# Kernel optimization log

Measured on AMD Instinct MI355X. Metric: run time of the kernel, lower is better.

Reference implementation:

```python
import jax, jax.numpy as jnp
import numpy as np

B, S, E = 2, 1024, 2048
NH = 8          # num attention heads
KVH = 1         # num key/value heads (GQA)
DH = E // NH    # head dim = 256
CAP = 15.0      # gate soft cap
EPS = 1e-6


def setup_inputs() -> dict:
    key = jax.random.key(0)
    ks = jax.random.split(key, 11)
    g = lambda k, shape, sc=0.02: (jax.random.normal(k, shape, jnp.float32) * sc)
    return {
        "x": jax.random.normal(ks[0], (B, S, E), jnp.float32),
        "Wq": g(ks[1], (E, NH * DH)),
        "Wk": g(ks[2], (E, KVH * DH)),
        "Wv": g(ks[3], (E, KVH * DH)),
        "Wog": g(ks[4], (E, E)),
        "Wi": g(ks[5], (E, NH)),
        "bi": g(ks[6], (NH,), 0.1),
        "Wf": g(ks[7], (E, NH)),
        "bf": jnp.ones((NH,), jnp.float32) * 2.0,  # bias forget gate open, as in xLSTM practice
        "gamma": jnp.ones((E,), jnp.float32),       # multihead layernorm weight
        "Wout": g(ks[8], (E, E)),
    }


def _soft_cap(z):
    return CAP * jnp.tanh(z / CAP)


def _repeat_kv(h, n_rep):
    # (B, KVH, S, DH) -> (B, KVH*n_rep, S, DH)
    if n_rep == 1:
        return h
    b, kvh, s, d = h.shape
    return jnp.broadcast_to(h[:, :, None], (b, kvh, n_rep, s, d)).reshape(b, kvh * n_rep, s, d)


def reference(x, Wq, Wk, Wv, Wog, Wi, bi, Wf, bf, gamma, Wout):
    # --- projections ---
    q = (x @ Wq).reshape(B, S, NH, DH).transpose(0, 2, 1, 3)          # (B,NH,S,DH)
    k = (x @ Wk).reshape(B, S, KVH, DH).transpose(0, 2, 1, 3)         # (B,KVH,S,DH)
    v = (x @ Wv).reshape(B, S, KVH, DH).transpose(0, 2, 1, 3)
    k = _repeat_kv(k, NH // KVH)
    v = _repeat_kv(v, NH // KVH)
    o_preact = x @ Wog                                                # (B,S,E)
    i_pre = _soft_cap(x @ Wi + bi).transpose(0, 2, 1)                 # (B,NH,S)
    f_pre = _soft_cap(x @ Wf + bf).transpose(0, 2, 1)                 # (B,NH,S)

    # --- parallel (stabilized) mLSTM backend ---
    logf = jax.nn.log_sigmoid(f_pre)
    cf = jnp.cumsum(logf, axis=-1)                                    # (B,NH,S)
    mat_logf = cf[:, :, :, None] - cf[:, :, None, :]                  # (B,NH,S,S)
    ltr = jnp.tril(jnp.ones((S, S), dtype=bool))
    mat_logD = jnp.where(ltr, mat_logf, -jnp.inf) + i_pre[:, :, None, :]
    vecM = jnp.max(mat_logD, axis=-1, keepdims=True)                  # (B,NH,S,1)
    matD = jnp.exp(mat_logD - vecM)
    matS = jnp.einsum('bhsd,bhtd->bhst', q, k) * (DH ** -0.5)
    matCt = matS * matD
    vecN = jnp.maximum(jnp.abs(matCt.sum(-1, keepdims=True)), jnp.exp(-vecM))
    matC = matCt / (vecN + EPS)
    h = jnp.einsum('bhst,bhtd->bhsd', matC, v)                        # (B,NH,S,DH)

    # --- multihead layernorm (per-head, float32 reductions) ---
    h = h.transpose(0, 2, 1, 3)                                       # (B,S,NH,DH)
    hf = h.astype(jnp.float32)
    mu = hf.mean(-1, keepdims=True)
    var = hf.var(-1, keepdims=True)
    h_norm = ((hf - mu) * jax.lax.rsqrt(var + EPS)).astype(h.dtype)
    h_norm = (h_norm * gamma.reshape(NH, DH)).reshape(B, S, E)

    # --- output gate + projection ---
    y = (jax.nn.sigmoid(o_preact) * h_norm) @ Wout
    return y
```

## Files before the change

kernel.cpp:

```cpp
#include <hip/hip_runtime.h>
#include <math.h>

#define S_LEN  1024
#define EMB    2048
#define NH_    8
#define DH_    256
#define TOKENS 2048
#define NBH    16
#define NQKVO  4608

typedef __attribute__((ext_vector_type(4))) float    f32x4;
typedef __attribute__((ext_vector_type(8))) _Float16 f16x8;
typedef __attribute__((ext_vector_type(4))) _Float16 f16x4;

__device__ __forceinline__ _Float16 f2h(float f) { return (_Float16)f; }

__device__ __forceinline__ void gload16(const void* g, void* l) {
  __builtin_amdgcn_global_load_lds(
      (const __attribute__((address_space(1))) void*)g,
      (__attribute__((address_space(3))) void*)l, 16, 0, 0);
}

__global__ __launch_bounds__(256) void prep_kernel(
    const float* __restrict__ x, const float* __restrict__ Wi, const float* __restrict__ bi,
    const float* __restrict__ Wf, const float* __restrict__ bfg,
    const float* __restrict__ Wq, const float* __restrict__ Wk,
    const float* __restrict__ Wv, const float* __restrict__ Wog,
    const float* __restrict__ Wout,
    _Float16* __restrict__ xh, float* __restrict__ ip, float* __restrict__ fp,
    _Float16* __restrict__ WcatT, _Float16* __restrict__ WoutT)
{
  __shared__ float shmem[64][65];
  int t = blockIdx.x;
  const int tid = threadIdx.x;
  if (t < TOKENS) {
    const int tok = t;
    const float* xr = x + (long)tok * EMB;
    float ai[8] = {}, af[8] = {};
    #pragma unroll
    for (int j = 0; j < 8; ++j) {
      const int e = tid + j * 256;
      const float xe = xr[e];
      xh[(long)tok * EMB + e] = f2h(xe);
      const float4* wi4 = (const float4*)(Wi + (long)e * 8);
      const float4* wf4 = (const float4*)(Wf + (long)e * 8);
      const float4 a0 = wi4[0], a1 = wi4[1], b0 = wf4[0], b1 = wf4[1];
      ai[0] += xe * a0.x; ai[1] += xe * a0.y; ai[2] += xe * a0.z; ai[3] += xe * a0.w;
      ai[4] += xe * a1.x; ai[5] += xe * a1.y; ai[6] += xe * a1.z; ai[7] += xe * a1.w;
      af[0] += xe * b0.x; af[1] += xe * b0.y; af[2] += xe * b0.z; af[3] += xe * b0.w;
      af[4] += xe * b1.x; af[5] += xe * b1.y; af[6] += xe * b1.z; af[7] += xe * b1.w;
    }
    #pragma unroll
    for (int hh = 0; hh < 8; ++hh)
      for (int off = 32; off; off >>= 1) {
        ai[hh] += __shfl_xor(ai[hh], off);
        af[hh] += __shfl_xor(af[hh], off);
      }
    float (*red)[16] = (float(*)[16])shmem;
    const int lane = tid & 63, wid = tid >> 6;
    if (lane == 0) {
      #pragma unroll
      for (int hh = 0; hh < 8; ++hh) { red[wid][hh] = ai[hh]; red[wid][hh + 8] = af[hh]; }
    }
    __syncthreads();
    if (tid < 16) {
      const float v = red[0][tid] + red[1][tid] + red[2][tid] + red[3][tid];
      const int b = tok >> 10, s = tok & 1023;
      if (tid < 8) {
        const float zv = v + bi[tid];
        ip[(long)(b * NH_ + tid) * S_LEN + s] = 15.0f * tanhf(zv * (1.0f / 15.0f));
      } else {
        const int hh = tid - 8;
        const float zv = v + bfg[hh];
        fp[(long)(b * NH_ + hh) * S_LEN + s] = 15.0f * tanhf(zv * (1.0f / 15.0f));
      }
    }
  } else {
    t -= TOKENS;
    const float* in; _Float16* out; int ldi, ct;
    if (t < 1024)      { in = Wq;   out = WcatT;                    ldi = 2048; ct = 32; }
    else if (t < 1152) { t -= 1024; in = Wk;  out = WcatT + (long)2048 * EMB; ldi = 256; ct = 4; }
    else if (t < 1280) { t -= 1152; in = Wv;  out = WcatT + (long)2304 * EMB; ldi = 256; ct = 4; }
    else if (t < 2304) { t -= 1280; in = Wog; out = WcatT + (long)2560 * EMB; ldi = 2048; ct = 32; }
    else               { t -= 2304; in = Wout; out = WoutT;         ldi = 2048; ct = 32; }
    const long c0 = (long)(t % ct) * 64, r0 = (long)(t / ct) * 64;
    const int lx = tid & 63, ly = tid >> 6;
    #pragma unroll
    for (int i = 0; i < 16; ++i)
      shmem[ly + i * 4][lx] = in[(r0 + ly + i * 4) * ldi + c0 + lx];
    __syncthreads();
    #pragma unroll
    for (int i = 0; i < 16; ++i)
      out[(c0 + ly + i * 4) * EMB + r0 + lx] = f2h(shmem[lx][ly + i * 4]);
  }
}

template<typename CT, int BM>
__global__ __launch_bounds__(256) void gemm_bt_kernel(
    const _Float16* __restrict__ Ag, const _Float16* __restrict__ Btg,
    CT* __restrict__ Cg, int K, int lda, int ldb, int ldc,
    long sA, long sB, long sC, int zdivB, int mtiles, int causal)
{
  constexpr int MR = BM / 32;
  __shared__ _Float16 As[3][BM * 32];
  __shared__ _Float16 Bs[3][128 * 32];
  const int tid = threadIdx.x;
  const int lane = tid & 63, wid = tid >> 6;
  const int cpx = gridDim.x >> 3;
  const int wg = ((int)blockIdx.x & 7) * cpx + ((int)blockIdx.x >> 3);
  const int m0 = (wg % mtiles) * BM;
  const int n0 = (wg / mtiles) * 128;
  const int z  = blockIdx.z;
  const _Float16* Ap = Ag + (long)z * sA + (long)m0 * lda;
  const _Float16* Bp = Btg + (long)(z / zdivB) * sB + (long)n0 * ldb;
  const int wr = wid >> 1, wc = wid & 1;
  const int lrow = lane & 15, kseg = lane >> 4;
  const int kl = causal ? ((m0 + BM < K) ? m0 + BM : K) : K;

  auto stage = [&](int b, int k0) {
    #pragma unroll
    for (int i = 0; i < BM / 64; ++i) {
      const int cbase = (i * 4 + wid) * 64;
      const int row = (cbase >> 2) + (lane >> 2);
      const int src = ((lane & 3) ^ ((row >> 1) & 3)) * 8;
      gload16(Ap + (long)row * lda + k0 + src, (char*)As[b] + cbase * 16);
    }
    #pragma unroll
    for (int i = 0; i < 2; ++i) {
      const int cbase = (i * 4 + wid) * 64;
      const int row = (cbase >> 2) + (lane >> 2);
      const int src = ((lane & 3) ^ ((row >> 1) & 3)) * 8;
      gload16(Bp + (long)row * ldb + k0 + src, (char*)Bs[b] + cbase * 16);
    }
  };

  const int nt = kl >> 5;
  f32x4 acc[MR][4] = {};
  stage(0, 0);
  if (nt > 1) stage(1, 32);
  for (int t = 0; t < nt; ++t) {
    if (t + 2 < nt) {
      stage((t + 2) % 3, (t + 2) * 32);
      if constexpr (BM == 128) asm volatile("s_waitcnt vmcnt(8)" ::: "memory");
      else                     asm volatile("s_waitcnt vmcnt(6)" ::: "memory");
    } else if (t + 1 < nt) {
      if constexpr (BM == 128) asm volatile("s_waitcnt vmcnt(4)" ::: "memory");
      else                     asm volatile("s_waitcnt vmcnt(3)" ::: "memory");
    } else {
      asm volatile("s_waitcnt vmcnt(0)" ::: "memory");
    }
    __builtin_amdgcn_s_barrier();
    __builtin_amdgcn_sched_barrier(0);
    const int buf = t % 3;
    f16x8 fa[MR], fb[4];
    #pragma unroll
    for (int m = 0; m < MR; ++m) {
      const int row = wr * (BM / 2) + m * 16 + lrow;
      fa[m] = *(const f16x8*)&As[buf][row * 32 + ((kseg ^ ((row >> 1) & 3)) << 3)];
    }
    #pragma unroll
    for (int n = 0; n < 4; ++n) {
      const int row = wc * 64 + n * 16 + lrow;
      fb[n] = *(const f16x8*)&Bs[buf][row * 32 + ((kseg ^ ((row >> 1) & 3)) << 3)];
    }
    #pragma unroll
    for (int m = 0; m < MR; ++m)
      #pragma unroll
      for (int n = 0; n < 4; ++n)
        acc[m][n] = __builtin_amdgcn_mfma_f32_16x16x32_f16(fa[m], fb[n], acc[m][n], 0, 0, 0);
    __builtin_amdgcn_s_barrier();
  }
  CT* Cp = Cg + (long)z * sC;
  #pragma unroll
  for (int m = 0; m < MR; ++m)
    #pragma unroll
    for (int n = 0; n < 4; ++n)
      #pragma unroll
      for (int i = 0; i < 4; ++i) {
        const int r = m0 + wr * (BM / 2) + m * 16 + kseg * 4 + i;
        const int c = n0 + wc * 64 + n * 16 + lrow;
        Cp[(long)r * ldc + c] = (CT)acc[m][n][i];
      }
}

__global__ __launch_bounds__(256) void mid_kernel(
    const _Float16* __restrict__ qkvo, _Float16* __restrict__ vt,
    const float* __restrict__ fp, const float* __restrict__ ip,
    float* __restrict__ aArr, float* __restrict__ mArr, float* __restrict__ vMArr)
{
  __shared__ float shmem[64][65];
  const int tid = threadIdx.x;
  int t = blockIdx.x;
  if (t < NBH) {
    const int bh = t;
    const int lane = tid & 63, wid = tid >> 6;
    float* wsum = &shmem[0][0];
    float* wmax = &shmem[1][0];
    const int s4 = tid * 4;
    const float4 fv = *(const float4*)(fp + (long)bh * S_LEN + s4);
    const float4 iv = *(const float4*)(ip + (long)bh * S_LEN + s4);
    float lg[4];
    lg[0] = fminf(fv.x, 0.0f) - log1pf(expf(-fabsf(fv.x)));
    lg[1] = fminf(fv.y, 0.0f) - log1pf(expf(-fabsf(fv.y)));
    lg[2] = fminf(fv.z, 0.0f) - log1pf(expf(-fabsf(fv.z)));
    lg[3] = fminf(fv.w, 0.0f) - log1pf(expf(-fabsf(fv.w)));
    float c0 = lg[0], c1 = c0 + lg[1], c2 = c1 + lg[2], c3 = c2 + lg[3];
    float ts = c3;
    #pragma unroll
    for (int off = 1; off < 64; off <<= 1) {
      const float o = __shfl_up(ts, off);
      if (lane >= off) ts += o;
    }
    const float texcl = ts - c3;
    if (lane == 63) wsum[wid] = ts;
    __syncthreads();
    float woff = 0.0f;
    for (int w = 0; w < wid; ++w) woff += wsum[w];
    const float base = woff + texcl;
    const float cf[4] = { base + c0, base + c1, base + c2, base + c3 };
    const float a[4] = { iv.x - cf[0], iv.y - cf[1], iv.z - cf[2], iv.w - cf[3] };
    float l0 = a[0], l1 = fmaxf(l0, a[1]), l2 = fmaxf(l1, a[2]), l3 = fmaxf(l2, a[3]);
    float incl = l3;
    #pragma unroll
    for (int off = 1; off < 64; off <<= 1) {
      const float o = __shfl_up(incl, off);
      if (lane >= off) incl = fmaxf(incl, o);
    }
    float excl = __shfl_up(incl, 1);
    if (lane == 0) excl = -3.0e38f;
    if (lane == 63) wmax[wid] = incl;
    __syncthreads();
    float wpre = -3.0e38f;
    for (int w = 0; w < wid; ++w) wpre = fmaxf(wpre, wmax[w]);
    const float pre = fmaxf(wpre, excl);
    float mm[4];
    mm[0] = fmaxf(pre, a[0]); mm[1] = fmaxf(mm[0], a[1]);
    mm[2] = fmaxf(mm[1], a[2]); mm[3] = fmaxf(mm[2], a[3]);
    float4 av = { a[0], a[1], a[2], a[3] };
    float4 mv = { mm[0], mm[1], mm[2], mm[3] };
    float4 vv = { cf[0] + mm[0], cf[1] + mm[1], cf[2] + mm[2], cf[3] + mm[3] };
    *(float4*)(aArr + (long)bh * S_LEN + s4) = av;
    *(float4*)(mArr + (long)bh * S_LEN + s4) = mv;
    *(float4*)(vMArr + (long)bh * S_LEN + s4) = vv;
  } else {
    t -= NBH;
    const int z = t >> 6, rem = t & 63;
    const long c0 = (long)(rem & 3) * 64;
    const long r0 = (long)(rem >> 2) * 64;
    const _Float16* ipt = qkvo + (long)z * S_LEN * NQKVO + 2304;
    _Float16* op = vt + (long)z * DH_ * S_LEN;
    const int lx = tid & 63, ly = tid >> 6;
    #pragma unroll
    for (int i = 0; i < 16; ++i)
      shmem[ly + i * 4][lx] = (float)ipt[(r0 + ly + i * 4) * NQKVO + c0 + lx];
    __syncthreads();
    #pragma unroll
    for (int i = 0; i < 16; ++i)
      op[(c0 + ly + i * 4) * S_LEN + r0 + lx] = f2h(shmem[lx][ly + i * 4]);
  }
}

__global__ __launch_bounds__(512) void att_fused_kernel(
    const _Float16* __restrict__ qkvo, const _Float16* __restrict__ vt,
    const float* __restrict__ aArr, const float* __restrict__ mArr,
    const float* __restrict__ vMArr, const float* __restrict__ gamma,
    _Float16* __restrict__ ub)
{
  __shared__ _Float16 Qs[2][32 * 256];
  __shared__ _Float16 Ws[2][32 * 128];
  __shared__ float nsh[2][8][32];
  __shared__ float s2sh[2][8][32];
  __shared__ float invs[2][32];
  __shared__ float musl[2][32], rssl[2][32];
  const int tid = threadIdx.x;
  const int lane = tid & 63, wid = tid >> 6;
  const int bh = blockIdx.y;
  const int b = bh >> 3, h = bh & 7;
  const int r0[2] = { (int)blockIdx.x * 32, (31 - (int)blockIdx.x) * 32 };
  const _Float16* Qg = qkvo + (long)(b * S_LEN) * NQKVO + h * DH_;
  const _Float16* Kg = qkvo + (long)(b * S_LEN) * NQKVO + 2048;
  const _Float16* Og = qkvo + (long)(b * S_LEN) * NQKVO + 2560 + h * DH_;
  const _Float16* Vt = vt + (long)b * DH_ * S_LEN;
  const float* aA = aArr + (long)bh * S_LEN;
  const float* mA = mArr + (long)bh * S_LEN;
  const float* gam = gamma + h * DH_;
  const int lrow = lane & 15, kseg = lane >> 4;
  const int tbase = 16 * wid;
  const int dbase = 32 * wid;

  #pragma unroll
  for (int i = 0; i < 4; ++i) {
    const int cbase = (i * 8 + wid) * 64;
    const int c = cbase + lane;
    const int sub = c >> 10, row = (c >> 5) & 31, slot = c & 31;
    gload16(Qg + (long)(r0[sub] + row) * NQKVO + (slot ^ (row & 7)) * 8,
            (char*)Qs + cbase * 16);
  }

  float m_s[2][2][4];
  #pragma unroll
  for (int sub = 0; sub < 2; ++sub)
    #pragma unroll
    for (int m = 0; m < 2; ++m)
      #pragma unroll
      for (int i = 0; i < 4; ++i)
        m_s[sub][m][i] = mA[r0[sub] + m * 16 + kseg * 4 + i];
  __syncthreads();

  f32x4 hacc[2][2][2] = {};
  float nacc[2][2][4] = {};
  for (int n0 = 0; n0 <= r0[1]; n0 += 128) {
    f32x4 acc[2][2] = {};
    f16x8 fb, fbn;
    fb = *(const f16x8*)(Kg + (long)(n0 + tbase + lrow) * NQKVO + kseg * 8);
    #pragma unroll
    for (int k0 = 0; k0 < DH_; k0 += 32) {
      if (k0 + 32 < DH_)
        fbn = *(const f16x8*)(Kg + (long)(n0 + tbase + lrow) * NQKVO + k0 + 32 + kseg * 8);
      const int chunk = (k0 >> 3) + kseg;
      __builtin_amdgcn_s_setprio(1);
      #pragma unroll
      for (int sub = 0; sub < 2; ++sub) {
        if (n0 > r0[sub]) continue;
        #pragma unroll
        for (int m = 0; m < 2; ++m) {
          const int qrow = m * 16 + lrow;
          const f16x8 fa = *(const f16x8*)&Qs[sub][qrow * 256 + ((chunk ^ (qrow & 7)) << 3)];
          acc[sub][m] = __builtin_amdgcn_mfma_f32_16x16x32_f16(fa, fb, acc[sub][m], 0, 0, 0);
        }
      }
      __builtin_amdgcn_s_setprio(0);
      fb = fbn;
    }
    const float a_t = aA[n0 + tbase + lrow];
    #pragma unroll
    for (int sub = 0; sub < 2; ++sub) {
      if (n0 > r0[sub]) continue;
      #pragma unroll
      for (int m = 0; m < 2; ++m)
        #pragma unroll
        for (int i = 0; i < 4; ++i) {
          const int sr = m * 16 + kseg * 4 + i;
          const int t  = tbase + lrow;
          float w = 0.0f;
          if (n0 + t <= r0[sub] + sr)
            w = acc[sub][m][i] * 0.0625f * expf(a_t - m_s[sub][m][i]);
          nacc[sub][m][i] += w;
          Ws[sub][sr * 128 + (((t >> 3) ^ ((sr & 7) << 1)) << 3) + (t & 7)] = f2h(w);
        }
    }
    f16x8 vb[2], vbn[2];
    #pragma unroll
    for (int n = 0; n < 2; ++n)
      vb[n] = *(const f16x8*)(Vt + (long)(dbase + n * 16 + lrow) * S_LEN + n0 + kseg * 8);
    __syncthreads();
    #pragma unroll
    for (int kt = 0; kt < 128; kt += 32) {
      if (kt + 32 < 128) {
        #pragma unroll
        for (int n = 0; n < 2; ++n)
          vbn[n] = *(const f16x8*)(Vt + (long)(dbase + n * 16 + lrow) * S_LEN + n0 + kt + 32 + kseg * 8);
      }
      const int chunk = (kt >> 3) + kseg;
      __builtin_amdgcn_s_setprio(1);
      #pragma unroll
      for (int sub = 0; sub < 2; ++sub) {
        if (n0 > r0[sub]) continue;
        #pragma unroll
        for (int m = 0; m < 2; ++m) {
          const int row = m * 16 + lrow;
          const f16x8 wa = *(const f16x8*)&Ws[sub][row * 128 + ((chunk ^ ((row & 7) << 1)) << 3)];
          #pragma unroll
          for (int n = 0; n < 2; ++n)
            hacc[sub][m][n] = __builtin_amdgcn_mfma_f32_16x16x32_f16(wa, vb[n], hacc[sub][m][n], 0, 0, 0);
        }
      }
      __builtin_amdgcn_s_setprio(0);
      vb[0] = vbn[0]; vb[1] = vbn[1];
    }
    __syncthreads();
  }
  #pragma unroll
  for (int sub = 0; sub < 2; ++sub)
    #pragma unroll
    for (int m = 0; m < 2; ++m)
      #pragma unroll
      for (int i = 0; i < 4; ++i) {
        float v = nacc[sub][m][i];
        v += __shfl_xor(v, 1); v += __shfl_xor(v, 2);
        v += __shfl_xor(v, 4); v += __shfl_xor(v, 8);
        if (lrow == 0) nsh[sub][wid][m * 16 + kseg * 4 + i] = v;
      }
  __syncthreads();
  if (tid < 64) {
    const int sub = tid >> 5, sr = tid & 31;
    float tot = 0.0f;
    #pragma unroll
    for (int w = 0; w < 8; ++w) tot += nsh[sub][w][sr];
    const float vm = vMArr[(long)bh * S_LEN + r0[sub] + sr];
    const float vecN = fmaxf(fabsf(tot), expf(-vm));
    invs[sub][sr] = 1.0f / (vecN + 1e-6f);
  }
  __syncthreads();
  #pragma unroll
  for (int sub = 0; sub < 2; ++sub)
    #pragma unroll
    for (int m = 0; m < 2; ++m)
      #pragma unroll
      for (int i = 0; i < 4; ++i) {
        const int row = m * 16 + kseg * 4 + i;
        const float inv = invs[sub][row];
        hacc[sub][m][0][i] *= inv;
        hacc[sub][m][1][i] *= inv;
        float s1 = hacc[sub][m][0][i] + hacc[sub][m][1][i];
        float s2 = hacc[sub][m][0][i] * hacc[sub][m][0][i]
                 + hacc[sub][m][1][i] * hacc[sub][m][1][i];
        s1 += __shfl_xor(s1, 1); s2 += __shfl_xor(s2, 1);
        s1 += __shfl_xor(s1, 2); s2 += __shfl_xor(s2, 2);
        s1 += __shfl_xor(s1, 4); s2 += __shfl_xor(s2, 4);
        s1 += __shfl_xor(s1, 8); s2 += __shfl_xor(s2, 8);
        if (lrow == 0) { nsh[sub][wid][row] = s1; s2sh[sub][wid][row] = s2; }
      }
  __syncthreads();
  if (tid < 64) {
    const int sub = tid >> 5, sr = tid & 31;
    float s1 = 0.0f, s2 = 0.0f;
    #pragma unroll
    for (int w = 0; w < 8; ++w) { s1 += nsh[sub][w][sr]; s2 += s2sh[sub][w][sr]; }
    const float mu = s1 * (1.0f / 256.0f);
    const float var = s2 * (1.0f / 256.0f) - mu * mu;
    musl[sub][sr] = mu;
    rssl[sub][sr] = rsqrtf(var + 1e-6f);
  }
  __syncthreads();
  #pragma unroll
  for (int sub = 0; sub < 2; ++sub)
    #pragma unroll
    for (int m = 0; m < 2; ++m)
      #pragma unroll
      for (int n = 0; n < 2; ++n)
        #pragma unroll
        for (int i = 0; i < 4; ++i) {
          const int row = m * 16 + kseg * 4 + i;
          const int d = dbase + n * 16 + lrow;
          const long gr = r0[sub] + row;
          const float hn = (hacc[sub][m][n][i] - musl[sub][row]) * rssl[sub][row] * gam[d];
          const float o = (float)Og[((long)gr) * NQKVO + d];
          ub[(long)(b * S_LEN + gr) * EMB + h * DH_ + d] =
              f2h(hn * (1.0f / (1.0f + expf(-o))));
        }
}

extern "C" void kernel_launch(void* const* d_in, const int* in_sizes, int n_in,
                              void* d_out, int out_size, void* d_ws, size_t ws_size,
                              hipStream_t stream)
{
  (void)in_sizes; (void)n_in; (void)out_size; (void)ws_size;
  const float* x     = (const float*)d_in[0];
  const float* Wq    = (const float*)d_in[1];
  const float* Wk    = (const float*)d_in[2];
  const float* Wv    = (const float*)d_in[3];
  const float* Wog   = (const float*)d_in[4];
  const float* Wi    = (const float*)d_in[5];
  const float* bi    = (const float*)d_in[6];
  const float* Wf    = (const float*)d_in[7];
  const float* bfg   = (const float*)d_in[8];
  const float* gamma = (const float*)d_in[9];
  const float* Wout  = (const float*)d_in[10];

  char* base = (char*)d_ws;
  size_t off = 0;
  auto take = [&](size_t bytes) -> char* {
    char* p = base + off;
    off += (bytes + 255) & ~(size_t)255;
    return p;
  };
  _Float16* xh    = (_Float16*)take((size_t)TOKENS * EMB * 2);
  _Float16* WcatT = (_Float16*)take((size_t)NQKVO * EMB * 2);
  _Float16* WoutT = (_Float16*)take((size_t)EMB * EMB * 2);
  _Float16* qkvo  = (_Float16*)take((size_t)TOKENS * NQKVO * 2);
  _Float16* vt    = (_Float16*)take((size_t)2 * DH_ * S_LEN * 2);
  _Float16* ub    = (_Float16*)take((size_t)TOKENS * EMB * 2);
  float*    ip    = (float*)take((size_t)NBH * S_LEN * 4);
  float*    fp    = (float*)take((size_t)NBH * S_LEN * 4);
  float*    aA    = (float*)take((size_t)NBH * S_LEN * 4);
  float*    mA    = (float*)take((size_t)NBH * S_LEN * 4);
  float*    vM    = (float*)take((size_t)NBH * S_LEN * 4);
  float*    y     = (float*)d_out;

  const dim3 blk(256);
  prep_kernel<<<dim3(TOKENS + 3328), blk, 0, stream>>>(
      x, Wi, bi, Wf, bfg, Wq, Wk, Wv, Wog, Wout, xh, ip, fp, WcatT, WoutT);
  gemm_bt_kernel<_Float16, 128><<<dim3(36 * 16), blk, 0, stream>>>(
      xh, WcatT, qkvo, EMB, EMB, EMB, NQKVO, 0L, 0L, 0L, 1, 16, 0);
  mid_kernel<<<dim3(NBH + 128), blk, 0, stream>>>(qkvo, vt, fp, ip, aA, mA, vM);
  att_fused_kernel<<<dim3(16, NBH), dim3(512), 0, stream>>>(
      qkvo, vt, aA, mA, vM, gamma, ub);
  gemm_bt_kernel<float, 64><<<dim3(32 * 16), blk, 0, stream>>>(
      ub, WoutT, y, EMB, EMB, EMB, EMB, 0L, 0L, 0L, 1, 32, 0);
}
```

Before: 175.3 us.

## Use 256x256-tile 512-thread GEMM kernel for fused QKV/gate projection

Adds a dedicated GEMM kernel with 256x256 output tiles and eight waves per block, each wave computing a 128x64 sub-tile, and uses it for the concatenated Q/K/V/output-gate projection. Larger tiles raise data reuse per LDS load and cut global traffic per FLOP. The trade-off is far fewer blocks (144) than compute units, which may leave much of the GPU idle. It also drops the unused batch/causal parameters from the existing GEMM and simplifies a max chain.

```diff
diff --git a/kernel.cpp b/kernel.cpp
--- a/kernel.cpp
+++ b/kernel.cpp
@@ -95,11 +95,91 @@
   }
 }
 
+template<typename CT>
+__global__ __launch_bounds__(512, 2) void gemm_bt256_kernel(
+    const _Float16* __restrict__ Ag, const _Float16* __restrict__ Btg,
+    CT* __restrict__ Cg, int K, int lda, int ldb, int ldc, int mtiles)
+{
+  __shared__ _Float16 As[3][256 * 32];
+  __shared__ _Float16 Bs[3][256 * 32];
+  const int tid = threadIdx.x;
+  const int lane = tid & 63, wid = tid >> 6;
+  const int cpx = gridDim.x >> 3;
+  const int wg = ((int)blockIdx.x & 7) * cpx + ((int)blockIdx.x >> 3);
+  const int m0 = (wg % mtiles) * 256;
+  const int n0 = (wg / mtiles) * 256;
+  const _Float16* Ap = Ag + (long)m0 * lda;
+  const _Float16* Bp = Btg + (long)n0 * ldb;
+  const int wr = wid >> 2, wc = wid & 3;
+  const int lrow = lane & 15, kseg = lane >> 4;
+
+  auto stage = [&](int b, int k0) {
+    #pragma unroll
+    for (int i = 0; i < 2; ++i) {
+      const int cbase = (i * 8 + wid) * 64;
+      const int row = (cbase >> 2) + (lane >> 2);
+      const int src = ((lane & 3) ^ ((row >> 1) & 3)) * 8;
+      gload16(Ap + (long)row * lda + k0 + src, (char*)As[b] + cbase * 16);
+    }
+    #pragma unroll
+    for (int i = 0; i < 2; ++i) {
+      const int cbase = (i * 8 + wid) * 64;
+      const int row = (cbase >> 2) + (lane >> 2);
+      const int src = ((lane & 3) ^ ((row >> 1) & 3)) * 8;
+      gload16(Bp + (long)row * ldb + k0 + src, (char*)Bs[b] + cbase * 16);
+    }
+  };
+
+  const int nt = K >> 5;
+  f32x4 acc[8][4] = {};
+  stage(0, 0);
+  if (nt > 1) stage(1, 32);
+  for (int t = 0; t < nt; ++t) {
+    if (t + 2 < nt) {
+      stage((t + 2) % 3, (t + 2) * 32);
+      asm volatile("s_waitcnt vmcnt(8)" ::: "memory");
+    } else if (t + 1 < nt) {
+      asm volatile("s_waitcnt vmcnt(4)" ::: "memory");
+    } else {
+      asm volatile("s_waitcnt vmcnt(0)" ::: "memory");
+    }
+    __builtin_amdgcn_s_barrier();
+    __builtin_amdgcn_sched_barrier(0);
+    const int buf = t % 3;
+    f16x8 fa[8], fb[4];
+    #pragma unroll
+    for (int m = 0; m < 8; ++m) {
+      const int row = wr * 128 + m * 16 + lrow;
+      fa[m] = *(const f16x8*)&As[buf][row * 32 + ((kseg ^ ((row >> 1) & 3)) << 3)];
+    }
+    #pragma unroll
+    for (int n = 0; n < 4; ++n) {
+      const int row = wc * 64 + n * 16 + lrow;
+      fb[n] = *(const f16x8*)&Bs[buf][row * 32 + ((kseg ^ ((row >> 1) & 3)) << 3)];
+    }
+    #pragma unroll
+    for (int m = 0; m < 8; ++m)
+      #pragma unroll
+      for (int n = 0; n < 4; ++n)
+        acc[m][n] = __builtin_amdgcn_mfma_f32_16x16x32_f16(fa[m], fb[n], acc[m][n], 0, 0, 0);
+    __builtin_amdgcn_s_barrier();
+  }
+  #pragma unroll
+  for (int m = 0; m < 8; ++m)
+    #pragma unroll
+    for (int n = 0; n < 4; ++n)
+      #pragma unroll
+      for (int i = 0; i < 4; ++i) {
+        const int r = m0 + wr * 128 + m * 16 + kseg * 4 + i;
+        const int c = n0 + wc * 64 + n * 16 + lrow;
+        Cg[(long)r * ldc + c] = (CT)acc[m][n][i];
+      }
+}
+
 template<typename CT, int BM>
 __global__ __launch_bounds__(256) void gemm_bt_kernel(
     const _Float16* __restrict__ Ag, const _Float16* __restrict__ Btg,
-    CT* __restrict__ Cg, int K, int lda, int ldb, int ldc,
-    long sA, long sB, long sC, int zdivB, int mtiles, int causal)
+    CT* __restrict__ Cg, int K, int lda, int ldb, int ldc, int mtiles)
 {
   constexpr int MR = BM / 32;
   __shared__ _Float16 As[3][BM * 32];
@@ -110,12 +190,10 @@
   const int wg = ((int)blockIdx.x & 7) * cpx + ((int)blockIdx.x >> 3);
   const int m0 = (wg % mtiles) * BM;
   const int n0 = (wg / mtiles) * 128;
-  const int z  = blockIdx.z;
-  const _Float16* Ap = Ag + (long)z * sA + (long)m0 * lda;
-  const _Float16* Bp = Btg + (long)(z / zdivB) * sB + (long)n0 * ldb;
+  const _Float16* Ap = Ag + (long)m0 * lda;
+  const _Float16* Bp = Btg + (long)n0 * ldb;
   const int wr = wid >> 1, wc = wid & 1;
   const int lrow = lane & 15, kseg = lane >> 4;
-  const int kl = causal ? ((m0 + BM < K) ? m0 + BM : K) : K;
 
   auto stage = [&](int b, int k0) {
     #pragma unroll
@@ -134,7 +212,7 @@
     }
   };
 
-  const int nt = kl >> 5;
+  const int nt = K >> 5;
   f32x4 acc[MR][4] = {};
   stage(0, 0);
   if (nt > 1) stage(1, 32);
@@ -170,7 +248,6 @@
         acc[m][n] = __builtin_amdgcn_mfma_f32_16x16x32_f16(fa[m], fb[n], acc[m][n], 0, 0, 0);
     __builtin_amdgcn_s_barrier();
   }
-  CT* Cp = Cg + (long)z * sC;
   #pragma unroll
   for (int m = 0; m < MR; ++m)
     #pragma unroll
@@ -179,7 +256,7 @@
       for (int i = 0; i < 4; ++i) {
         const int r = m0 + wr * (BM / 2) + m * 16 + kseg * 4 + i;
         const int c = n0 + wc * 64 + n * 16 + lrow;
-        Cp[(long)r * ldc + c] = (CT)acc[m][n][i];
+        Cg[(long)r * ldc + c] = (CT)acc[m][n][i];
       }
 }
 
@@ -219,7 +296,7 @@
     const float base = woff + texcl;
     const float cf[4] = { base + c0, base + c1, base + c2, base + c3 };
     const float a[4] = { iv.x - cf[0], iv.y - cf[1], iv.z - cf[2], iv.w - cf[3] };
-    float l0 = a[0], l1 = fmaxf(l0, a[1]), l2 = fmaxf(l1, a[2]), l3 = fmaxf(l2, a[3]);
+    float l1 = fmaxf(a[0], a[1]), l3 = fmaxf(fmaxf(l1, a[2]), a[3]);
     float incl = l3;
     #pragma unroll
     for (int off = 1; off < 64; off <<= 1) {
@@ -491,11 +568,11 @@
   const dim3 blk(256);
   prep_kernel<<<dim3(TOKENS + 3328), blk, 0, stream>>>(
       x, Wi, bi, Wf, bfg, Wq, Wk, Wv, Wog, Wout, xh, ip, fp, WcatT, WoutT);
-  gemm_bt_kernel<_Float16, 128><<<dim3(36 * 16), blk, 0, stream>>>(
-      xh, WcatT, qkvo, EMB, EMB, EMB, NQKVO, 0L, 0L, 0L, 1, 16, 0);
+  gemm_bt256_kernel<_Float16><<<dim3(8 * 18), dim3(512), 0, stream>>>(
+      xh, WcatT, qkvo, EMB, EMB, EMB, NQKVO, 8);
   mid_kernel<<<dim3(NBH + 128), blk, 0, stream>>>(qkvo, vt, fp, ip, aA, mA, vM);
   att_fused_kernel<<<dim3(16, NBH), dim3(512), 0, stream>>>(
       qkvo, vt, aA, mA, vM, gamma, ub);
   gemm_bt_kernel<float, 64><<<dim3(32 * 16), blk, 0, stream>>>(
-      ub, WoutT, y, EMB, EMB, EMB, EMB, 0L, 0L, 0L, 1, 32, 0);
-}
+      ub, WoutT, y, EMB, EMB, EMB, EMB, 32);
+}
```

Measured after the change: 194.6 us. 1.11x slower.

## Fold input/forget gate projections into the fused QKVO GEMM

Applied to the files above, without the earlier changes.

Moves the x@Wi and x@Wf gate projections out of the prep kernel's per-token scalar reduction and appends them as 16 extra columns (padded to 128) of the fp16 QKVO GEMM weight matrix. The mid kernel now applies the bias and soft cap itself, reading the gate preactivations from the qkvo buffer. The token part of prep becomes a pure vectorized fp16 conversion. The cost is one extra 128-wide GEMM column tile, mostly zero padding, and gate preactivations now computed with fp16 inputs and stored in fp16, which lowers their precision.

```diff
diff --git a/kernel.cpp b/kernel.cpp
--- a/kernel.cpp
+++ b/kernel.cpp
@@ -7,7 +7,7 @@
 #define DH_    256
 #define TOKENS 2048
 #define NBH    16
-#define NQKVO  4608
+#define NQKVO  4736
 
 typedef __attribute__((ext_vector_type(4))) float    f32x4;
 typedef __attribute__((ext_vector_type(8))) _Float16 f16x8;
@@ -22,60 +22,25 @@
 }
 
 __global__ __launch_bounds__(256) void prep_kernel(
-    const float* __restrict__ x, const float* __restrict__ Wi, const float* __restrict__ bi,
-    const float* __restrict__ Wf, const float* __restrict__ bfg,
+    const float* __restrict__ x,
     const float* __restrict__ Wq, const float* __restrict__ Wk,
     const float* __restrict__ Wv, const float* __restrict__ Wog,
     const float* __restrict__ Wout,
-    _Float16* __restrict__ xh, float* __restrict__ ip, float* __restrict__ fp,
+    const float* __restrict__ Wi, const float* __restrict__ Wf,
+    _Float16* __restrict__ xh,
     _Float16* __restrict__ WcatT, _Float16* __restrict__ WoutT)
 {
   __shared__ float shmem[64][65];
   int t = blockIdx.x;
   const int tid = threadIdx.x;
   if (t < TOKENS) {
-    const int tok = t;
-    const float* xr = x + (long)tok * EMB;
-    float ai[8] = {}, af[8] = {};
-    #pragma unroll
-    for (int j = 0; j < 8; ++j) {
-      const int e = tid + j * 256;
-      const float xe = xr[e];
-      xh[(long)tok * EMB + e] = f2h(xe);
-      const float4* wi4 = (const float4*)(Wi + (long)e * 8);
-      const float4* wf4 = (const float4*)(Wf + (long)e * 8);
-      const float4 a0 = wi4[0], a1 = wi4[1], b0 = wf4[0], b1 = wf4[1];
-      ai[0] += xe * a0.x; ai[1] += xe * a0.y; ai[2] += xe * a0.z; ai[3] += xe * a0.w;
-      ai[4] += xe * a1.x; ai[5] += xe * a1.y; ai[6] += xe * a1.z; ai[7] += xe * a1.w;
-      af[0] += xe * b0.x; af[1] += xe * b0.y; af[2] += xe * b0.z; af[3] += xe * b0.w;
-      af[4] += xe * b1.x; af[5] += xe * b1.y; af[6] += xe * b1.z; af[7] += xe * b1.w;
-    }
-    #pragma unroll
-    for (int hh = 0; hh < 8; ++hh)
-      for (int off = 32; off; off >>= 1) {
-        ai[hh] += __shfl_xor(ai[hh], off);
-        af[hh] += __shfl_xor(af[hh], off);
-      }
-    float (*red)[16] = (float(*)[16])shmem;
-    const int lane = tid & 63, wid = tid >> 6;
-    if (lane == 0) {
-      #pragma unroll
-      for (int hh = 0; hh < 8; ++hh) { red[wid][hh] = ai[hh]; red[wid][hh + 8] = af[hh]; }
-    }
-    __syncthreads();
-    if (tid < 16) {
-      const float v = red[0][tid] + red[1][tid] + red[2][tid] + red[3][tid];
-      const int b = tok >> 10, s = tok & 1023;
-      if (tid < 8) {
-        const float zv = v + bi[tid];
-        ip[(long)(b * NH_ + tid) * S_LEN + s] = 15.0f * tanhf(zv * (1.0f / 15.0f));
-      } else {
-        const int hh = tid - 8;
-        const float zv = v + bfg[hh];
-        fp[(long)(b * NH_ + hh) * S_LEN + s] = 15.0f * tanhf(zv * (1.0f / 15.0f));
-      }
-    }
-  } else {
+    const long base = (long)t * EMB + tid * 8;
+    const float4 a = *(const float4*)(x + base);
+    const float4 b = *(const float4*)(x + base + 4);
+    f16x8 o = {f2h(a.x), f2h(a.y), f2h(a.z), f2h(a.w),
+               f2h(b.x), f2h(b.y), f2h(b.z), f2h(b.w)};
+    *(f16x8*)(xh + base) = o;
+  } else if (t < TOKENS + 3328) {
     t -= TOKENS;
     const float* in; _Float16* out; int ldi, ct;
     if (t < 1024)      { in = Wq;   out = WcatT;                    ldi = 2048; ct = 32; }
@@ -92,14 +57,30 @@
     #pragma unroll
     for (int i = 0; i < 16; ++i)
       out[(c0 + ly + i * 4) * EMB + r0 + lx] = f2h(shmem[lx][ly + i * 4]);
+  } else {
+    const int j = t - (TOKENS + 3328);
+    const int row = 4608 + j * 2 + (tid >> 7);
+    const int c0 = (tid & 127) * 16;
+    _Float16* dst = WcatT + (long)row * EMB + c0;
+    if (row < 4616) {
+      const int jj = row - 4608;
+      #pragma unroll
+      for (int k = 0; k < 16; ++k) dst[k] = f2h(Wi[(long)(c0 + k) * 8 + jj]);
+    } else if (row < 4624) {
+      const int jj = row - 4616;
+      #pragma unroll
+      for (int k = 0; k < 16; ++k) dst[k] = f2h(Wf[(long)(c0 + k) * 8 + jj]);
+    } else {
+      #pragma unroll
+      for (int k = 0; k < 16; ++k) dst[k] = (_Float16)0.0f;
+    }
   }
 }
 
 template<typename CT, int BM>
 __global__ __launch_bounds__(256) void gemm_bt_kernel(
     const _Float16* __restrict__ Ag, const _Float16* __restrict__ Btg,
-    CT* __restrict__ Cg, int K, int lda, int ldb, int ldc,
-    long sA, long sB, long sC, int zdivB, int mtiles, int causal)
+    CT* __restrict__ Cg, int K, int lda, int ldb, int ldc, int mtiles)
 {
   constexpr int MR = BM / 32;
   __shared__ _Float16 As[3][BM * 32];
@@ -110,12 +91,10 @@
   const int wg = ((int)blockIdx.x & 7) * cpx + ((int)blockIdx.x >> 3);
   const int m0 = (wg % mtiles) * BM;
   const int n0 = (wg / mtiles) * 128;
-  const int z  = blockIdx.z;
-  const _Float16* Ap = Ag + (long)z * sA + (long)m0 * lda;
-  const _Float16* Bp = Btg + (long)(z / zdivB) * sB + (long)n0 * ldb;
+  const _Float16* Ap = Ag + (long)m0 * lda;
+  const _Float16* Bp = Btg + (long)n0 * ldb;
   const int wr = wid >> 1, wc = wid & 1;
   const int lrow = lane & 15, kseg = lane >> 4;
-  const int kl = causal ? ((m0 + BM < K) ? m0 + BM : K) : K;
 
   auto stage = [&](int b, int k0) {
     #pragma unroll
@@ -134,7 +113,7 @@
     }
   };
 
-  const int nt = kl >> 5;
+  const int nt = K >> 5;
   f32x4 acc[MR][4] = {};
   stage(0, 0);
   if (nt > 1) stage(1, 32);
@@ -170,7 +149,6 @@
         acc[m][n] = __builtin_amdgcn_mfma_f32_16x16x32_f16(fa[m], fb[n], acc[m][n], 0, 0, 0);
     __builtin_amdgcn_s_barrier();
   }
-  CT* Cp = Cg + (long)z * sC;
   #pragma unroll
   for (int m = 0; m < MR; ++m)
     #pragma unroll
@@ -179,13 +157,13 @@
       for (int i = 0; i < 4; ++i) {
         const int r = m0 + wr * (BM / 2) + m * 16 + kseg * 4 + i;
         const int c = n0 + wc * 64 + n * 16 + lrow;
-        Cp[(long)r * ldc + c] = (CT)acc[m][n][i];
+        Cg[(long)r * ldc + c] = (CT)acc[m][n][i];
       }
 }
 
 __global__ __launch_bounds__(256) void mid_kernel(
     const _Float16* __restrict__ qkvo, _Float16* __restrict__ vt,
-    const float* __restrict__ fp, const float* __restrict__ ip,
+    const float* __restrict__ bi, const float* __restrict__ bfg,
     float* __restrict__ aArr, float* __restrict__ mArr, float* __restrict__ vMArr)
 {
   __shared__ float shmem[64][65];
@@ -193,17 +171,23 @@
   int t = blockIdx.x;
   if (t < NBH) {
     const int bh = t;
+    const int b = bh >> 3, h = bh & 7;
     const int lane = tid & 63, wid = tid >> 6;
     float* wsum = &shmem[0][0];
     float* wmax = &shmem[1][0];
+    const float bih = bi[h], bfh = bfg[h];
     const int s4 = tid * 4;
-    const float4 fv = *(const float4*)(fp + (long)bh * S_LEN + s4);
-    const float4 iv = *(const float4*)(ip + (long)bh * S_LEN + s4);
+    const _Float16* zb = qkvo + (long)(b * S_LEN + s4) * NQKVO;
+    float zf[4], zi[4];
+    #pragma unroll
+    for (int k = 0; k < 4; ++k) {
+      zi[k] = 15.0f * tanhf(((float)zb[(long)k * NQKVO + 4608 + h] + bih) * (1.0f / 15.0f));
+      zf[k] = 15.0f * tanhf(((float)zb[(long)k * NQKVO + 4616 + h] + bfh) * (1.0f / 15.0f));
+    }
     float lg[4];
-    lg[0] = fminf(fv.x, 0.0f) - log1pf(expf(-fabsf(fv.x)));
-    lg[1] = fminf(fv.y, 0.0f) - log1pf(expf(-fabsf(fv.y)));
-    lg[2] = fminf(fv.z, 0.0f) - log1pf(expf(-fabsf(fv.z)));
-    lg[3] = fminf(fv.w, 0.0f) - log1pf(expf(-fabsf(fv.w)));
+    #pragma unroll
+    for (int k = 0; k < 4; ++k)
+      lg[k] = fminf(zf[k], 0.0f) - log1pf(expf(-fabsf(zf[k])));
     float c0 = lg[0], c1 = c0 + lg[1], c2 = c1 + lg[2], c3 = c2 + lg[3];
     float ts = c3;
     #pragma unroll
@@ -218,8 +202,8 @@
     for (int w = 0; w < wid; ++w) woff += wsum[w];
     const float base = woff + texcl;
     const float cf[4] = { base + c0, base + c1, base + c2, base + c3 };
-    const float a[4] = { iv.x - cf[0], iv.y - cf[1], iv.z - cf[2], iv.w - cf[3] };
-    float l0 = a[0], l1 = fmaxf(l0, a[1]), l2 = fmaxf(l1, a[2]), l3 = fmaxf(l2, a[3]);
+    const float a[4] = { zi[0] - cf[0], zi[1] - cf[1], zi[2] - cf[2], zi[3] - cf[3] };
+    float l1 = fmaxf(a[0], a[1]), l3 = fmaxf(fmaxf(l1, a[2]), a[3]);
     float incl = l3;
     #pragma unroll
     for (int off = 1; off < 64; off <<= 1) {
@@ -481,21 +465,19 @@
   _Float16* qkvo  = (_Float16*)take((size_t)TOKENS * NQKVO * 2);
   _Float16* vt    = (_Float16*)take((size_t)2 * DH_ * S_LEN * 2);
   _Float16* ub    = (_Float16*)take((size_t)TOKENS * EMB * 2);
-  float*    ip    = (float*)take((size_t)NBH * S_LEN * 4);
-  float*    fp    = (float*)take((size_t)NBH * S_LEN * 4);
   float*    aA    = (float*)take((size_t)NBH * S_LEN * 4);
   float*    mA    = (float*)take((size_t)NBH * S_LEN * 4);
   float*    vM    = (float*)take((size_t)NBH * S_LEN * 4);
   float*    y     = (float*)d_out;
 
   const dim3 blk(256);
-  prep_kernel<<<dim3(TOKENS + 3328), blk, 0, stream>>>(
-      x, Wi, bi, Wf, bfg, Wq, Wk, Wv, Wog, Wout, xh, ip, fp, WcatT, WoutT);
-  gemm_bt_kernel<_Float16, 128><<<dim3(36 * 16), blk, 0, stream>>>(
-      xh, WcatT, qkvo, EMB, EMB, EMB, NQKVO, 0L, 0L, 0L, 1, 16, 0);
-  mid_kernel<<<dim3(NBH + 128), blk, 0, stream>>>(qkvo, vt, fp, ip, aA, mA, vM);
+  prep_kernel<<<dim3(TOKENS + 3328 + 64), blk, 0, stream>>>(
+      x, Wq, Wk, Wv, Wog, Wout, Wi, Wf, xh, WcatT, WoutT);
+  gemm_bt_kernel<_Float16, 128><<<dim3(16 * 37), blk, 0, stream>>>(
+      xh, WcatT, qkvo, EMB, EMB, EMB, NQKVO, 16);
+  mid_kernel<<<dim3(NBH + 128), blk, 0, stream>>>(qkvo, vt, bi, bfg, aA, mA, vM);
   att_fused_kernel<<<dim3(16, NBH), dim3(512), 0, stream>>>(
       qkvo, vt, aA, mA, vM, gamma, ub);
   gemm_bt_kernel<float, 64><<<dim3(32 * 16), blk, 0, stream>>>(
-      ub, WoutT, y, EMB, EMB, EMB, EMB, 0L, 0L, 0L, 1, 32, 0);
-}
+      ub, WoutT, y, EMB, EMB, EMB, EMB, 32);
+}
```

Result: faster. 167.2 us (-4.6%).
